# Kernel tuning notes

Measured on AMD Instinct MI355X. Metric: run time of the kernel, lower is better.

The kernel has to match this reference:

```python
import jax, jax.numpy as jnp
import numpy as np

B, S, H, MODES = 16, 8192, 256, 16

def setup_inputs() -> dict:
    key = jax.random.key(0)
    k1, k2, k3 = jax.random.split(key, 3)
    x = jax.random.normal(k1, (B, S, H), dtype=jnp.float32)
    # complex weights ~ 0.02 * randn (real and imag parts kept as floats)
    w_real = jax.random.normal(k2, (H, H, MODES), dtype=jnp.float32) * 0.02
    w_imag = jax.random.normal(k3, (H, H, MODES), dtype=jnp.float32) * 0.02
    return {"x": x, "w_real": w_real, "w_imag": w_imag}

def reference(x, w_real, w_imag):
    batch, seq_len, hidden = x.shape
    x_ft = jnp.fft.rfft(x, axis=1)                      # [B, F, H] complex64, F = S//2 + 1
    m = min(MODES, x_ft.shape[1])
    w = (w_real + 1j * w_imag)[:, :, :m]                # [H, K, m]
    # batched complex matmul over the kept modes (replaces per-mode loop)
    out_modes = jnp.einsum('bmh,hkm->bmk', x_ft[:, :m, :], w)
    out_ft = jnp.zeros_like(x_ft).at[:, :m, :].set(out_modes)
    y = jnp.fft.irfft(out_ft, n=seq_len, axis=1)        # [B, S, H] float32
    return jax.nn.gelu(y, approximate=False)            # torch nn.GELU default = exact erf
```

## Files before the change

kernel.cpp:

```cpp
#include <hip/hip_runtime.h>
#include <math.h>

#define BB 16
#define SS 8192
#define HH 256
#define MM 16
#define DNC 64
#define DL 128
#define SCH 16
#define SNC 129
#define QOFF (BB * MM * 2 * HH)


__global__ __launch_bounds__(256) void k_pre(const float* __restrict__ wr,
                                             const float* __restrict__ wi,
                                             float* __restrict__ T,
                                             float* __restrict__ Wtr,
                                             float* __restrict__ Wti) {
    const int t = threadIdx.x;
    if (blockIdx.x < 512) {
        int idx = blockIdx.x * 256 + t;
        int s = idx >> 4, k = idx & 15;
        int r = (k * s) & (SS - 1);
        float th = (float)r * (6.28318530717958647692f / (float)SS);
        float sn, cn;
        sincosf(th, &sn, &cn);
        T[s * 32 + 2 * k]     = cn;
        T[s * 32 + 2 * k + 1] = sn;
    } else {
        __shared__ float lds[4096 + 256];
        int bid = blockIdx.x - 512;
        int h = bid & 255, y = bid >> 8;
        const float* src = (y == 0 ? wr : wi) + (size_t)h * 4096;
        float* dst = (y == 0 ? Wtr : Wti);
#pragma unroll
        for (int j = 0; j < 16; j++) {
            int i = j * 256 + t;
            lds[i + (i >> 4)] = src[i];
        }
        __syncthreads();
#pragma unroll
        for (int m = 0; m < 16; m++) {
            int i = t * 16 + m;
            dst[(size_t)m * (HH * HH) + (size_t)h * HH + t] = lds[i + (i >> 4)];
        }
    }
}

__device__ __forceinline__ float fast_gelu(float y) {
    float x  = fabsf(y) * 0.70710678118654752f;
    float t  = __builtin_amdgcn_rcpf(fmaf(0.3275911f, x, 1.0f));
    float e  = __expf(-x * x);
    float p  = fmaf(fmaf(fmaf(fmaf(1.061405429f, t, -1.453152027f), t,
                   1.421413741f), t, -0.284496736f), t, 0.254829592f) * t;
    float erfabs = fmaf(-p, e, 1.0f);
    return fmaf(0.5f * fabsf(y), erfabs, 0.5f * y);
}

__global__ __launch_bounds__(256) void k_dft(const float* __restrict__ x,
                                             const float* __restrict__ T,
                                             float* __restrict__ Xp) {
    const int c = blockIdx.x, b = blockIdx.y, t = threadIdx.x;
    const int s0 = c * DL;
    const float* xp = x + ((size_t)b * SS + s0) * HH + t;
    const float* tw = T + (size_t)s0 * 32;

    float cs[MM], sn[MM];
#pragma unroll
    for (int k = 0; k < MM; k++) { cs[k] = 0.f; sn[k] = 0.f; }

    float xv[4], xn[4];
#pragma unroll
    for (int q = 0; q < 4; q++) xv[q] = xp[(size_t)q * HH];

    auto compute4 = [&](int i, const float* xq) {
#pragma unroll
        for (int q = 0; q < 4; q++) {
            const float4* t4 = (const float4*)(tw + (size_t)(i + q) * 32);
            float xval = xq[q];
#pragma unroll
            for (int j = 0; j < 8; j++) {
                float4 tt = t4[j];
                cs[2 * j]     = fmaf(tt.x, xval, cs[2 * j]);
                sn[2 * j]     = fmaf(tt.y, xval, sn[2 * j]);
                cs[2 * j + 1] = fmaf(tt.z, xval, cs[2 * j + 1]);
                sn[2 * j + 1] = fmaf(tt.w, xval, sn[2 * j + 1]);
            }
        }
    };

#pragma unroll 2
    for (int i = 0; i < DL - 4; i += 4) {
#pragma unroll
        for (int q = 0; q < 4; q++)
            xn[q] = xp[(size_t)(i + 4 + q) * HH];
        compute4(i, xv);
#pragma unroll
        for (int q = 0; q < 4; q++) xv[q] = xn[q];
    }
    compute4(DL - 4, xv);

    size_t base = ((size_t)(b * DNC + c) * MM) * (2 * HH) + t;
#pragma unroll
    for (int k = 0; k < MM; k++) {
        Xp[base + (size_t)k * (2 * HH)]      = cs[k];
        Xp[base + (size_t)k * (2 * HH) + HH] = sn[k];
    }
}

__global__ __launch_bounds__(256) void k_mix(const float* __restrict__ Xp,
                                             const float* __restrict__ Wtr,
                                             const float* __restrict__ Wti,
                                             float* __restrict__ ABp) {
    const int m = blockIdx.x, b = blockIdx.y, q = blockIdx.z, t = threadIdx.x;
    const int h0 = q * 128;
    __shared__ float tmp[2][2][128];
    __shared__ float xr_s[128], xs_s[128];

    {
        int hh = t & 127, ph = t >> 7;
        float s0 = 0.f, s1 = 0.f;
        size_t base = (((size_t)b * DNC + ph * 32) * MM + m) * (2 * HH) + h0 + hh;
        const size_t ps = (size_t)MM * 2 * HH;
#pragma unroll 4
        for (int p = 0; p < 32; p++) {
            s0 += Xp[base + (size_t)p * ps];
            s1 += Xp[base + (size_t)p * ps + HH];
        }
        tmp[ph][0][hh] = s0;
        tmp[ph][1][hh] = s1;
        __syncthreads();
        if (t < 128) {
            xr_s[t] = tmp[0][0][t] + tmp[1][0][t];
            xs_s[t] = tmp[0][1][t] + tmp[1][1][t];
        }
        __syncthreads();
    }

    const float* wr_m = Wtr + (size_t)m * (HH * HH) + (size_t)h0 * HH;
    const float* wi_m = Wti + (size_t)m * (HH * HH) + (size_t)h0 * HH;
    float re = 0.f, im = 0.f;
#pragma unroll 8
    for (int hh = 0; hh < 128; hh++) {
        float a  = wr_m[(size_t)hh * HH + t];
        float bw = wi_m[(size_t)hh * HH + t];
        float xr = xr_s[hh];
        float xs = xs_s[hh];
        re = fmaf(xr, a, re);  re = fmaf(xs, bw, re);
        im = fmaf(xr, bw, im); im = fmaf(-xs, a, im);
    }
    float scale = (m == 0 ? 1.f : 2.f) / (float)SS;
    size_t o = (size_t)q * QOFF + (((size_t)b * MM + m) * 2) * HH + t;
    ABp[o]      = scale * re;
    ABp[o + HH] = -scale * im;
}

__global__ __launch_bounds__(256) void k_synth(const float* __restrict__ ABp,
                                               const float* __restrict__ T,
                                               float* __restrict__ out) {
    const int c = blockIdx.x, b = blockIdx.y, h = threadIdx.x;
    float a[MM], bc[MM];
#pragma unroll
    for (int k = 0; k < MM; k++) {
        size_t o = (((size_t)b * MM + k) * 2) * HH + h;
        a[k]  = ABp[o]      + ABp[o + QOFF];
        bc[k] = ABp[o + HH] + ABp[o + HH + QOFF];
    }
    const int nv = (c == SNC - 1) ? 1 : SCH;
    const int v0 = c * SCH;
    float* ob = out + (size_t)b * SS * HH + h;

#pragma unroll 2
    for (int i = 0; i < nv; i++) {
        int v = v0 + i;
        const float4* tw4 = (const float4*)(T + (size_t)v * 32);
        float Pe = 0.f, Po = 0.f, Qe = 0.f, Qo = 0.f;
#pragma unroll
        for (int j = 0; j < 8; j++) {
            float4 t = tw4[j];
            Pe = fmaf(a[2 * j],      t.x, Pe);
            Qe = fmaf(bc[2 * j],     t.y, Qe);
            Po = fmaf(a[2 * j + 1],  t.z, Po);
            Qo = fmaf(bc[2 * j + 1], t.w, Qo);
        }
        float Pp = Pe + Po, Pm = Pe - Po, Qp = Qe + Qo, Qm = Qe - Qo;
        ob[(size_t)v * HH]                        = fast_gelu(Pp + Qp);
        ob[(size_t)(SS / 2 - v) * HH]             = fast_gelu(Pm - Qm);
        ob[(size_t)(SS / 2 + v) * HH]             = fast_gelu(Pm + Qm);
        ob[(size_t)((SS - v) & (SS - 1)) * HH]    = fast_gelu(Pp - Qp);
    }
}

extern "C" void kernel_launch(void* const* d_in, const int* in_sizes, int n_in,
                              void* d_out, int out_size, void* d_ws, size_t ws_size,
                              hipStream_t stream) {
    const float* x   = (const float*)d_in[0];
    const float* w_r = (const float*)d_in[1];
    const float* w_i = (const float*)d_in[2];
    float* out = (float*)d_out;
    float* ws  = (float*)d_ws;

    float* T   = ws;
    float* ABp = ws + 262144;
    float* Xp  = out;
    float* Wtr = out + (size_t)16 * 1024 * 1024;
    float* Wti = out + (size_t)17 * 1024 * 1024;

    hipLaunchKernelGGL(k_pre,   dim3(1024), dim3(256), 0, stream, w_r, w_i, T, Wtr, Wti);
    hipLaunchKernelGGL(k_dft,   dim3(DNC, BB), dim3(256), 0, stream, x, T, Xp);
    hipLaunchKernelGGL(k_mix,   dim3(MM, BB, 2), dim3(256), 0, stream, Xp, Wtr, Wti, ABp);
    hipLaunchKernelGGL(k_synth, dim3(SNC, BB), dim3(256), 0, stream, ABp, T, out);
}
```

Baseline: 123.4 us.

## Retile DFT kernel so each wave owns four modes and lanes own four channels

The forward DFT kernel now gives each of the four waves a group of four modes, and each lane handles four consecutive hidden channels loaded as float4. Before, every thread computed all sixteen modes for a single channel. Each twiddle load is now reused across four channels, and the x loads and Xp stores become 128-bit vectors. In exchange, each x row is read by all four waves (four times per block, mostly served from cache), and the launch bound now asks for four blocks per CU.

New measurement: 141.7 us. +14.9%, slower.

```diff
diff --git a/kernel.cpp b/kernel.cpp
--- a/kernel.cpp
+++ b/kernel.cpp
@@ -57,54 +57,48 @@
     return fmaf(0.5f * fabsf(y), erfabs, 0.5f * y);
 }
 
-__global__ __launch_bounds__(256) void k_dft(const float* __restrict__ x,
-                                             const float* __restrict__ T,
-                                             float* __restrict__ Xp) {
+__global__ __launch_bounds__(256, 4) void k_dft(const float* __restrict__ x,
+                                                const float* __restrict__ T,
+                                                float* __restrict__ Xp) {
     const int c = blockIdx.x, b = blockIdx.y, t = threadIdx.x;
+    const int w = t >> 6, l = t & 63;
     const int s0 = c * DL;
-    const float* xp = x + ((size_t)b * SS + s0) * HH + t;
-    const float* tw = T + (size_t)s0 * 32;
-
-    float cs[MM], sn[MM];
-#pragma unroll
-    for (int k = 0; k < MM; k++) { cs[k] = 0.f; sn[k] = 0.f; }
-
-    float xv[4], xn[4];
-#pragma unroll
-    for (int q = 0; q < 4; q++) xv[q] = xp[(size_t)q * HH];
-
-    auto compute4 = [&](int i, const float* xq) {
+    const float* xp = x + ((size_t)b * SS + s0) * HH + 4 * l;
+    const float* tw = T + (size_t)s0 * 32 + 8 * w;
+
+    float cs[4][4], sn[4][4];
+#pragma unroll
+    for (int k = 0; k < 4; k++)
+#pragma unroll
+        for (int q = 0; q < 4; q++) { cs[k][q] = 0.f; sn[k][q] = 0.f; }
+
+#pragma unroll 4
+    for (int i = 0; i < DL; i++) {
+        float4 xv = *(const float4*)(xp + (size_t)i * HH);
+        float4 t0 = *(const float4*)(tw + (size_t)i * 32);
+        float4 t1 = *(const float4*)(tw + (size_t)i * 32 + 4);
+        const float xq[4] = { xv.x, xv.y, xv.z, xv.w };
 #pragma unroll
         for (int q = 0; q < 4; q++) {
-            const float4* t4 = (const float4*)(tw + (size_t)(i + q) * 32);
-            float xval = xq[q];
-#pragma unroll
-            for (int j = 0; j < 8; j++) {
-                float4 tt = t4[j];
-                cs[2 * j]     = fmaf(tt.x, xval, cs[2 * j]);
-                sn[2 * j]     = fmaf(tt.y, xval, sn[2 * j]);
-                cs[2 * j + 1] = fmaf(tt.z, xval, cs[2 * j + 1]);
-                sn[2 * j + 1] = fmaf(tt.w, xval, sn[2 * j + 1]);
-            }
-        }
-    };
-
-#pragma unroll 2
-    for (int i = 0; i < DL - 4; i += 4) {
-#pragma unroll
-        for (int q = 0; q < 4; q++)
-            xn[q] = xp[(size_t)(i + 4 + q) * HH];
-        compute4(i, xv);
-#pragma unroll
-        for (int q = 0; q < 4; q++) xv[q] = xn[q];
-    }
-    compute4(DL - 4, xv);
-
-    size_t base = ((size_t)(b * DNC + c) * MM) * (2 * HH) + t;
-#pragma unroll
-    for (int k = 0; k < MM; k++) {
-        Xp[base + (size_t)k * (2 * HH)]      = cs[k];
-        Xp[base + (size_t)k * (2 * HH) + HH] = sn[k];
+            cs[0][q] = fmaf(t0.x, xq[q], cs[0][q]);
+            sn[0][q] = fmaf(t0.y, xq[q], sn[0][q]);
+            cs[1][q] = fmaf(t0.z, xq[q], cs[1][q]);
+            sn[1][q] = fmaf(t0.w, xq[q], sn[1][q]);
+            cs[2][q] = fmaf(t1.x, xq[q], cs[2][q]);
+            sn[2][q] = fmaf(t1.y, xq[q], sn[2][q]);
+            cs[3][q] = fmaf(t1.z, xq[q], cs[3][q]);
+            sn[3][q] = fmaf(t1.w, xq[q], sn[3][q]);
+        }
+    }
+
+    size_t base = ((size_t)(b * DNC + c) * MM) * (2 * HH) + 4 * l;
+#pragma unroll
+    for (int kk = 0; kk < 4; kk++) {
+        int k = 4 * w + kk;
+        *(float4*)(Xp + base + (size_t)k * (2 * HH)) =
+            make_float4(cs[kk][0], cs[kk][1], cs[kk][2], cs[kk][3]);
+        *(float4*)(Xp + base + (size_t)k * (2 * HH) + HH) =
+            make_float4(sn[kk][0], sn[kk][1], sn[kk][2], sn[kk][3]);
     }
 }
 
```
